# Kernel optimization log

Measured on AMD Instinct MI355X. Metric: run time of the kernel, lower is better.

The kernel has to match this reference:

```python
import jax, jax.numpy as jnp
import numpy as np

EPS = 1e-5
QB = 127.0  # 2**(8-1) - 1


def absmean_quantize(w):
    """Ternary quantization (BitNet b1.58): gamma = mean|W|, W_q in {-1,0,1}."""
    gamma = jnp.mean(jnp.abs(w))
    u = w / jnp.maximum(gamma, EPS)
    w_q = jnp.clip(jnp.round(u), -1.0, 1.0)
    return w_q, gamma


def absmax_quantize(x, bits=8):
    """Per-token int8 absmax quantization: alpha = max|x| over last dim."""
    qb = float(2 ** (bits - 1) - 1)
    alpha = jnp.max(jnp.abs(x), axis=-1, keepdims=True)  # [..., 1]
    u = x * qb / jnp.maximum(alpha, EPS)
    x_q = jnp.clip(jnp.round(u), -qb, qb)
    return x_q, alpha


def setup_inputs() -> dict:
    key = jax.random.key(0)
    k1, k2 = jax.random.split(key)
    B, S, D_IN, D_OUT = 4, 2048, 2048, 8192
    x = jax.random.normal(k1, (B, S, D_IN), dtype=jnp.float32)
    # kaiming-uniform-ish init scale for weight [out, in]
    bound = 1.0 / np.sqrt(D_IN)
    weight = jax.random.uniform(k2, (D_OUT, D_IN), minval=-bound, maxval=bound, dtype=jnp.float32)
    return {"x": x, "weight": weight}


def reference(x, weight):
    w_q, gamma = absmean_quantize(weight)          # [O,I], scalar
    x_q, alpha = absmax_quantize(x, bits=8)        # [B,S,I], [B,S,1]
    out = jnp.einsum('bsi,oi->bso', x_q, w_q)      # float matmul of quantized values
    scale = alpha * gamma / QB                     # [B,S,1]
    return out * scale
```

## Files before the change

### kernel.cpp

```cpp
#include <hip/hip_runtime.h>
#include <hip/hip_bf16.h>
#include <stdint.h>

typedef int i32x4 __attribute__((ext_vector_type(4)));

#define K_DIM 2048
#define M_DIM 8192
#define N_DIM 8192
#define QBF   127.0f
#define EPSF  1e-5f
#define NT    32

__device__ __forceinline__ void load_lds16(const void* gsrc, void* ldst) {
    __builtin_amdgcn_global_load_lds(
        (__attribute__((address_space(1))) void*)gsrc,
        (__attribute__((address_space(3))) void*)ldst,
        16, 0, 0);
}

__global__ __launch_bounds__(256) void k_abs_partial(const float* __restrict__ w,
                                                     float* __restrict__ partial) {
    __shared__ float red[256];
    int t = threadIdx.x, b = blockIdx.x;
    const float4* w4 = (const float4*)w;
    size_t base = (size_t)b * 2048;
    float s = 0.f;
#pragma unroll
    for (int j = 0; j < 8; ++j) {
        float4 v = w4[base + j * 256 + t];
        s += fabsf(v.x) + fabsf(v.y) + fabsf(v.z) + fabsf(v.w);
    }
    red[t] = s; __syncthreads();
    for (int off = 128; off > 0; off >>= 1) {
        if (t < off) red[t] += red[t + off];
        __syncthreads();
    }
    if (t == 0) partial[b] = red[0];
}

__global__ __launch_bounds__(256) void k_gamma(const float* __restrict__ partial,
                                               float* __restrict__ gamma) {
    __shared__ float red[256];
    int t = threadIdx.x;
    float s = 0.f;
#pragma unroll
    for (int j = 0; j < 8; ++j) s += partial[t + j * 256];
    red[t] = s; __syncthreads();
    for (int off = 128; off > 0; off >>= 1) {
        if (t < off) red[t] += red[t + off];
        __syncthreads();
    }
    if (t == 0) gamma[0] = red[0] / 16777216.0f;
}

__global__ __launch_bounds__(256) void k_quant_w(const float* __restrict__ w,
                                                 const float* __restrict__ gamma,
                                                 uint* __restrict__ wq) {
    float g = fmaxf(gamma[0], EPSF);
    int tid = blockIdx.x * 256 + threadIdx.x;
    float4 v = ((const float4*)w)[tid];
    int a = (int)fminf(fmaxf(rintf(v.x / g), -1.f), 1.f);
    int b = (int)fminf(fmaxf(rintf(v.y / g), -1.f), 1.f);
    int c = (int)fminf(fmaxf(rintf(v.z / g), -1.f), 1.f);
    int d = (int)fminf(fmaxf(rintf(v.w / g), -1.f), 1.f);
    wq[tid] = (a & 255) | ((b & 255) << 8) | ((c & 255) << 16) | ((d & 255) << 24);
}

__global__ __launch_bounds__(256) void k_quant_x(const float* __restrict__ x,
                                                 uint* __restrict__ xq,
                                                 float* __restrict__ alpha) {
    __shared__ float red[256];
    int t = threadIdx.x, row = blockIdx.x;
    const float4* x4 = (const float4*)x + (size_t)row * 512;
    float4 v0 = x4[t], v1 = x4[t + 256];
    float m = fmaxf(fmaxf(fabsf(v0.x), fabsf(v0.y)), fmaxf(fabsf(v0.z), fabsf(v0.w)));
    m = fmaxf(m, fmaxf(fmaxf(fabsf(v1.x), fabsf(v1.y)), fmaxf(fabsf(v1.z), fabsf(v1.w))));
    red[t] = m; __syncthreads();
    for (int off = 128; off > 0; off >>= 1) {
        if (t < off) red[t] = fmaxf(red[t], red[t + off]);
        __syncthreads();
    }
    float a = red[0];
    if (t == 0) alpha[row] = a;
    float den = fmaxf(a, EPSF);
    uint* q = xq + (size_t)row * 512;
    int q0 = (int)fminf(fmaxf(rintf(v0.x * QBF / den), -QBF), QBF);
    int q1 = (int)fminf(fmaxf(rintf(v0.y * QBF / den), -QBF), QBF);
    int q2 = (int)fminf(fmaxf(rintf(v0.z * QBF / den), -QBF), QBF);
    int q3 = (int)fminf(fmaxf(rintf(v0.w * QBF / den), -QBF), QBF);
    q[t] = (q0 & 255) | ((q1 & 255) << 8) | ((q2 & 255) << 16) | ((q3 & 255) << 24);
    q0 = (int)fminf(fmaxf(rintf(v1.x * QBF / den), -QBF), QBF);
    q1 = (int)fminf(fmaxf(rintf(v1.y * QBF / den), -QBF), QBF);
    q2 = (int)fminf(fmaxf(rintf(v1.z * QBF / den), -QBF), QBF);
    q3 = (int)fminf(fmaxf(rintf(v1.w * QBF / den), -QBF), QBF);
    q[t + 256] = (q0 & 255) | ((q1 & 255) << 8) | ((q2 & 255) << 16) | ((q3 & 255) << 24);
}

__global__ __launch_bounds__(256, 2) void k_gemm(const uint8_t* __restrict__ xq,
                                                 const uint8_t* __restrict__ wq,
                                                 const float* __restrict__ alpha,
                                                 const float* __restrict__ gamma,
                                                 float* __restrict__ out) {
    __shared__ __align__(16) char smem[73728];

    int bid = blockIdx.x;
    int wg = (bid & 7) * 256 + (bid >> 3);
    int tm = wg >> 6, tn = wg & 63;

    int t = threadIdx.x;
    int w = t >> 6, l = t & 63;
    int wr = w >> 1, wc = w & 1;

    const uint8_t* srcb[6];
    int dstq[6];
    {
        int rsub = l >> 2;
        int clog = (l & 3) ^ ((rsub >> 1) & 3);
#pragma unroll
        for (int j = 0; j < 6; ++j) {
            int q = w * 6 + j;
            int isB = q >> 4;
            int r = (isB ? (q & 7) : q) * 16 + rsub;
            int grow = isB ? tn * 128 + r : tm * 256 + r;
            srcb[j] = (isB ? wq : xq) + (size_t)grow * K_DIM + clog * 16;
            dstq[j] = q * 1024;
        }
    }

    i32x4 acc[8][4];
#pragma unroll
    for (int m = 0; m < 8; ++m)
#pragma unroll
        for (int n = 0; n < 4; ++n) acc[m][n] = (i32x4){0, 0, 0, 0};

    int lrow = l & 15, kgrp = l >> 4;
    int cph = (kgrp ^ ((lrow >> 1) & 3)) * 16;
    int aoff[8], boff[4];
#pragma unroll
    for (int mf = 0; mf < 8; ++mf) aoff[mf] = (wr * 128 + mf * 16 + lrow) * 64 + cph;
#pragma unroll
    for (int nf = 0; nf < 4; ++nf) boff[nf] = 16384 + (wc * 64 + nf * 16 + lrow) * 64 + cph;

#pragma unroll
    for (int p = 0; p < 2; ++p)
#pragma unroll
        for (int j = 0; j < 6; ++j)
            load_lds16(srcb[j] + (size_t)p * 64, smem + p * 24576 + dstq[j]);

    int slot = 0;
    for (int kt = 0; kt < NT; ++kt) {
        char* sb = smem + slot * 24576;
        if (kt < NT - 1) asm volatile("s_waitcnt vmcnt(6)" ::: "memory");
        else             asm volatile("s_waitcnt vmcnt(0)" ::: "memory");
        __builtin_amdgcn_s_barrier();

        i32x4 a[8], b[4];
#pragma unroll
        for (int mf = 0; mf < 4; ++mf) a[mf] = *(const i32x4*)(sb + aoff[mf]);
#pragma unroll
        for (int nf = 0; nf < 4; ++nf) b[nf] = *(const i32x4*)(sb + boff[nf]);
        __builtin_amdgcn_sched_barrier(0);
        if (kt + 2 < NT) {
            int ds = slot + 2; if (ds >= 3) ds -= 3;
            char* db = smem + ds * 24576;
#pragma unroll
            for (int j = 0; j < 6; ++j)
                load_lds16(srcb[j] + (size_t)(kt + 2) * 64, db + dstq[j]);
        }
        __builtin_amdgcn_sched_barrier(0);
#pragma unroll
        for (int mf = 4; mf < 8; ++mf) a[mf] = *(const i32x4*)(sb + aoff[mf]);

        asm volatile("s_waitcnt lgkmcnt(4)" ::: "memory");
        __builtin_amdgcn_sched_barrier(0);
        __builtin_amdgcn_s_setprio(1);
#pragma unroll
        for (int mf = 0; mf < 4; ++mf)
#pragma unroll
            for (int nf = 0; nf < 4; ++nf)
                acc[mf][nf] = __builtin_amdgcn_mfma_i32_16x16x64_i8(
                    a[mf], b[nf], acc[mf][nf], 0, 0, 0);
        __builtin_amdgcn_s_setprio(0);

        asm volatile("s_waitcnt lgkmcnt(0)" ::: "memory");
        __builtin_amdgcn_sched_barrier(0);
        __builtin_amdgcn_s_setprio(1);
#pragma unroll
        for (int mf = 4; mf < 8; ++mf)
#pragma unroll
            for (int nf = 0; nf < 4; ++nf)
                acc[mf][nf] = __builtin_amdgcn_mfma_i32_16x16x64_i8(
                    a[mf], b[nf], acc[mf][nf], 0, 0, 0);
        __builtin_amdgcn_s_setprio(0);

        slot = (slot == 2) ? 0 : slot + 1;
    }

    float gs = gamma[0] / QBF;
    int orow0 = tm * 256 + wr * 128 + kgrp * 4;
    int ocol = tn * 128 + wc * 64 + lrow;
#pragma unroll
    for (int mf = 0; mf < 8; ++mf)
#pragma unroll
        for (int r = 0; r < 4; ++r) {
            int row = orow0 + mf * 16 + r;
            float s = alpha[row] * gs;
            size_t rb = (size_t)row * N_DIM + ocol;
#pragma unroll
            for (int nf = 0; nf < 4; ++nf)
                out[rb + nf * 16] = (float)acc[mf][nf][r] * s;
        }
}

extern "C" void kernel_launch(void* const* d_in, const int* in_sizes, int n_in,
                              void* d_out, int out_size, void* d_ws, size_t ws_size,
                              hipStream_t stream) {
    const float* x  = (const float*)d_in[0];
    const float* wt = (const float*)d_in[1];
    float* out = (float*)d_out;

    char* ws = (char*)d_ws;
    uint8_t* xq     = (uint8_t*)ws;
    uint8_t* wq     = (uint8_t*)(ws + 16777216);
    float* alpha    = (float*)(ws + 33554432);
    float* partial  = (float*)(ws + 33587200);
    float* gamma    = (float*)(ws + 33595392);

    k_abs_partial<<<2048, 256, 0, stream>>>(wt, partial);
    k_gamma<<<1, 256, 0, stream>>>(partial, gamma);
    k_quant_w<<<16384, 256, 0, stream>>>(wt, gamma, (uint*)wq);
    k_quant_x<<<8192, 256, 0, stream>>>(x, (uint*)xq, alpha);
    k_gemm<<<2048, 256, 0, stream>>>(xq, wq, alpha, gamma, out);
}
```

Before: 222.1 us.

## Prefetch next k-tile LDS fragments into registers during current MFMAs

After: 221.1 us, median of 3. Within noise of the previous version (-0.5%).

```diff
diff --git a/kernel.cpp b/kernel.cpp
--- a/kernel.cpp
+++ b/kernel.cpp
@@ -141,60 +141,81 @@
 #pragma unroll
     for (int nf = 0; nf < 4; ++nf) boff[nf] = 16384 + (wc * 64 + nf * 16 + lrow) * 64 + cph;
 
+    i32x4 ALe[4], BBe[4], ALo[4], BBo[4], AH[4];
+
 #pragma unroll
     for (int p = 0; p < 2; ++p)
 #pragma unroll
         for (int j = 0; j < 6; ++j)
             load_lds16(srcb[j] + (size_t)p * 64, smem + p * 24576 + dstq[j]);
-
-    int slot = 0;
-    for (int kt = 0; kt < NT; ++kt) {
-        char* sb = smem + slot * 24576;
-        if (kt < NT - 1) asm volatile("s_waitcnt vmcnt(6)" ::: "memory");
-        else             asm volatile("s_waitcnt vmcnt(0)" ::: "memory");
-        __builtin_amdgcn_s_barrier();
-
-        i32x4 a[8], b[4];
-#pragma unroll
-        for (int mf = 0; mf < 4; ++mf) a[mf] = *(const i32x4*)(sb + aoff[mf]);
-#pragma unroll
-        for (int nf = 0; nf < 4; ++nf) b[nf] = *(const i32x4*)(sb + boff[nf]);
-        __builtin_amdgcn_sched_barrier(0);
-        if (kt + 2 < NT) {
-            int ds = slot + 2; if (ds >= 3) ds -= 3;
-            char* db = smem + ds * 24576;
-#pragma unroll
-            for (int j = 0; j < 6; ++j)
-                load_lds16(srcb[j] + (size_t)(kt + 2) * 64, db + dstq[j]);
-        }
-        __builtin_amdgcn_sched_barrier(0);
-#pragma unroll
-        for (int mf = 4; mf < 8; ++mf) a[mf] = *(const i32x4*)(sb + aoff[mf]);
-
-        asm volatile("s_waitcnt lgkmcnt(4)" ::: "memory");
-        __builtin_amdgcn_sched_barrier(0);
-        __builtin_amdgcn_s_setprio(1);
-#pragma unroll
-        for (int mf = 0; mf < 4; ++mf)
-#pragma unroll
-            for (int nf = 0; nf < 4; ++nf)
-                acc[mf][nf] = __builtin_amdgcn_mfma_i32_16x16x64_i8(
-                    a[mf], b[nf], acc[mf][nf], 0, 0, 0);
-        __builtin_amdgcn_s_setprio(0);
-
-        asm volatile("s_waitcnt lgkmcnt(0)" ::: "memory");
-        __builtin_amdgcn_sched_barrier(0);
-        __builtin_amdgcn_s_setprio(1);
-#pragma unroll
-        for (int mf = 4; mf < 8; ++mf)
-#pragma unroll
-            for (int nf = 0; nf < 4; ++nf)
-                acc[mf][nf] = __builtin_amdgcn_mfma_i32_16x16x64_i8(
-                    a[mf], b[nf], acc[mf][nf], 0, 0, 0);
-        __builtin_amdgcn_s_setprio(0);
-
-        slot = (slot == 2) ? 0 : slot + 1;
-    }
+    asm volatile("s_waitcnt vmcnt(6)" ::: "memory");
+    __builtin_amdgcn_s_barrier();
+#pragma unroll
+    for (int mf = 0; mf < 4; ++mf) ALe[mf] = *(const i32x4*)(smem + aoff[mf]);
+#pragma unroll
+    for (int nf = 0; nf < 4; ++nf) BBe[nf] = *(const i32x4*)(smem + boff[nf]);
+    asm volatile("s_waitcnt lgkmcnt(0)" ::: "memory");
+    __builtin_amdgcn_sched_barrier(0);
+
+    int sl = 0;
+
+#define ITER(KT, ALC, BBC, ALN, BBN)                                         \
+    {                                                                        \
+        asm volatile("s_waitcnt vmcnt(0)" ::: "memory");    \
+        __builtin_amdgcn_s_barrier();                                        \
+        int s1 = sl + 1; if (s1 >= 3) s1 = 0;                                \
+        int s2 = s1 + 1; if (s2 >= 3) s2 = 0;                                \
+        char* sb  = smem + sl * 24576;                                       \
+        char* sbn = smem + s1 * 24576;                                       \
+        if ((KT) + 2 < NT) {                                                 \
+            char* db = smem + s2 * 24576;                                    \
+            _Pragma("unroll")                                                \
+            for (int j = 0; j < 6; ++j)                                      \
+                load_lds16(srcb[j] + (size_t)((KT) + 2) * 64, db + dstq[j]); \
+        }                                                                    \
+        _Pragma("unroll")                                                    \
+        for (int mf = 0; mf < 4; ++mf)                                       \
+            AH[mf] = *(const i32x4*)(sb + aoff[mf + 4]);                     \
+        if ((KT) + 1 < NT) {                                                 \
+            _Pragma("unroll")                                                \
+            for (int mf = 0; mf < 4; ++mf)                                   \
+                ALN[mf] = *(const i32x4*)(sbn + aoff[mf]);                   \
+            _Pragma("unroll")                                                \
+            for (int nf = 0; nf < 4; ++nf)                                   \
+                BBN[nf] = *(const i32x4*)(sbn + boff[nf]);                   \
+        }                                                                    \
+        __builtin_amdgcn_sched_barrier(0);                                   \
+        __builtin_amdgcn_s_setprio(1);                                       \
+        _Pragma("unroll")                                                    \
+        for (int mf = 0; mf < 4; ++mf)                                       \
+            _Pragma("unroll")                                                \
+            for (int nf = 0; nf < 4; ++nf)                                   \
+                acc[mf][nf] = __builtin_amdgcn_mfma_i32_16x16x64_i8(         \
+                    ALC[mf], BBC[nf], acc[mf][nf], 0, 0, 0);                 \
+        __builtin_amdgcn_s_setprio(0);                                       \
+        if ((KT) + 1 < NT)                                                   \
+            asm volatile("s_waitcnt lgkmcnt(8)" ::: "memory");               \
+        else                                                                 \
+            asm volatile("s_waitcnt lgkmcnt(0)" ::: "memory");               \
+        __builtin_amdgcn_sched_barrier(0);                                   \
+        __builtin_amdgcn_s_setprio(1);                                       \
+        _Pragma("unroll")                                                    \
+        for (int mf = 0; mf < 4; ++mf)                                       \
+            _Pragma("unroll")                                                \
+            for (int nf = 0; nf < 4; ++nf)                                   \
+                acc[mf + 4][nf] = __builtin_amdgcn_mfma_i32_16x16x64_i8(     \
+                    AH[mf], BBC[nf], acc[mf + 4][nf], 0, 0, 0);              \
+        __builtin_amdgcn_s_setprio(0);                                       \
+        asm volatile("s_waitcnt lgkmcnt(0)" ::: "memory");   \
+        __builtin_amdgcn_sched_barrier(0);                                   \
+        sl = s1;                                                             \
+    }
+
+    for (int kt = 0; kt < NT; kt += 2) {
+        ITER(kt,     ALe, BBe, ALo, BBo)
+        ITER(kt + 1, ALo, BBo, ALe, BBe)
+    }
+#undef ITER
 
     float gs = gamma[0] / QBF;
     int orow0 = tm * 256 + wr * 128 + kgrp * 4;
```

## Enlarge GEMM tile to 256x256 with per-wave private LDS double buffering

Applied to the files above, without the earlier changes.

Measured after the change: 220.5 us. Within noise of the previous version (-0.7%).

```diff
diff --git a/kernel.cpp b/kernel.cpp
--- a/kernel.cpp
+++ b/kernel.cpp
@@ -96,82 +96,80 @@
     q[t + 256] = (q0 & 255) | ((q1 & 255) << 8) | ((q2 & 255) << 16) | ((q3 & 255) << 24);
 }
 
-__global__ __launch_bounds__(256, 2) void k_gemm(const uint8_t* __restrict__ xq,
+__global__ __launch_bounds__(256, 1) void k_gemm(const uint8_t* __restrict__ xq,
                                                  const uint8_t* __restrict__ wq,
                                                  const float* __restrict__ alpha,
                                                  const float* __restrict__ gamma,
                                                  float* __restrict__ out) {
-    __shared__ __align__(16) char smem[73728];
+    __shared__ __align__(16) char smem[131072];
 
     int bid = blockIdx.x;
-    int wg = (bid & 7) * 256 + (bid >> 3);
-    int tm = wg >> 6, tn = wg & 63;
+    int wg = (bid & 7) * 128 + (bid >> 3);
+    int tm = wg >> 5, tn = wg & 31;
 
     int t = threadIdx.x;
     int w = t >> 6, l = t & 63;
     int wr = w >> 1, wc = w & 1;
-
-    const uint8_t* srcb[6];
-    int dstq[6];
+    char* wbase = smem + w * 32768;
+
+    const uint8_t* srcb[16];
     {
         int rsub = l >> 2;
         int clog = (l & 3) ^ ((rsub >> 1) & 3);
 #pragma unroll
-        for (int j = 0; j < 6; ++j) {
-            int q = w * 6 + j;
-            int isB = q >> 4;
-            int r = (isB ? (q & 7) : q) * 16 + rsub;
-            int grow = isB ? tn * 128 + r : tm * 256 + r;
+        for (int j = 0; j < 16; ++j) {
+            int isB = j >> 3;
+            int r = (j & 7) * 16 + rsub;
+            int grow = isB ? tn * 256 + wc * 128 + r
+                           : tm * 256 + wr * 128 + r;
             srcb[j] = (isB ? wq : xq) + (size_t)grow * K_DIM + clog * 16;
-            dstq[j] = q * 1024;
         }
     }
 
-    i32x4 acc[8][4];
+    i32x4 acc[8][8];
 #pragma unroll
     for (int m = 0; m < 8; ++m)
 #pragma unroll
-        for (int n = 0; n < 4; ++n) acc[m][n] = (i32x4){0, 0, 0, 0};
+        for (int n = 0; n < 8; ++n) acc[m][n] = (i32x4){0, 0, 0, 0};
 
     int lrow = l & 15, kgrp = l >> 4;
     int cph = (kgrp ^ ((lrow >> 1) & 3)) * 16;
-    int aoff[8], boff[4];
-#pragma unroll
-    for (int mf = 0; mf < 8; ++mf) aoff[mf] = (wr * 128 + mf * 16 + lrow) * 64 + cph;
-#pragma unroll
-    for (int nf = 0; nf < 4; ++nf) boff[nf] = 16384 + (wc * 64 + nf * 16 + lrow) * 64 + cph;
-
-#pragma unroll
-    for (int p = 0; p < 2; ++p)
-#pragma unroll
-        for (int j = 0; j < 6; ++j)
-            load_lds16(srcb[j] + (size_t)p * 64, smem + p * 24576 + dstq[j]);
-
-    int slot = 0;
-    for (int kt = 0; kt < NT; ++kt) {
-        char* sb = smem + slot * 24576;
-        if (kt < NT - 1) asm volatile("s_waitcnt vmcnt(6)" ::: "memory");
-        else             asm volatile("s_waitcnt vmcnt(0)" ::: "memory");
-        __builtin_amdgcn_s_barrier();
-
-        i32x4 a[8], b[4];
+    int aoff[8], boff[8];
+#pragma unroll
+    for (int mf = 0; mf < 8; ++mf) aoff[mf] = (mf * 16 + lrow) * 64 + cph;
+#pragma unroll
+    for (int nf = 0; nf < 8; ++nf) boff[nf] = 8192 + (nf * 16 + lrow) * 64 + cph;
+
+#pragma unroll
+    for (int j = 0; j < 16; ++j)
+        load_lds16(srcb[j], wbase + j * 1024);
+
+    for (int s = 0; s < NT; ++s) {
+        char* sb = wbase + (s & 1) * 16384;
+        if (s + 1 < NT) {
+            char* db = wbase + ((s + 1) & 1) * 16384;
+#pragma unroll
+            for (int j = 0; j < 16; ++j)
+                load_lds16(srcb[j] + (size_t)(s + 1) * 64, db + j * 1024);
+            asm volatile("s_waitcnt vmcnt(16)" ::: "memory");
+        } else {
+            asm volatile("s_waitcnt vmcnt(0)" ::: "memory");
+        }
+        __builtin_amdgcn_sched_barrier(0);
+
+        i32x4 a[8], b[8];
+#pragma unroll
+        for (int nf = 0; nf < 4; ++nf) b[nf] = *(const i32x4*)(sb + boff[nf]);
 #pragma unroll
         for (int mf = 0; mf < 4; ++mf) a[mf] = *(const i32x4*)(sb + aoff[mf]);
-#pragma unroll
-        for (int nf = 0; nf < 4; ++nf) b[nf] = *(const i32x4*)(sb + boff[nf]);
-        __builtin_amdgcn_sched_barrier(0);
-        if (kt + 2 < NT) {
-            int ds = slot + 2; if (ds >= 3) ds -= 3;
-            char* db = smem + ds * 24576;
-#pragma unroll
-            for (int j = 0; j < 6; ++j)
-                load_lds16(srcb[j] + (size_t)(kt + 2) * 64, db + dstq[j]);
-        }
         __builtin_amdgcn_sched_barrier(0);
 #pragma unroll
         for (int mf = 4; mf < 8; ++mf) a[mf] = *(const i32x4*)(sb + aoff[mf]);
-
-        asm volatile("s_waitcnt lgkmcnt(4)" ::: "memory");
+        __builtin_amdgcn_sched_barrier(0);
+#pragma unroll
+        for (int nf = 4; nf < 8; ++nf) b[nf] = *(const i32x4*)(sb + boff[nf]);
+
+        asm volatile("s_waitcnt lgkmcnt(8)" ::: "memory");
         __builtin_amdgcn_sched_barrier(0);
         __builtin_amdgcn_s_setprio(1);
 #pragma unroll
@@ -182,7 +180,7 @@
                     a[mf], b[nf], acc[mf][nf], 0, 0, 0);
         __builtin_amdgcn_s_setprio(0);
 
-        asm volatile("s_waitcnt lgkmcnt(0)" ::: "memory");
+        asm volatile("s_waitcnt lgkmcnt(4)" ::: "memory");
         __builtin_amdgcn_sched_barrier(0);
         __builtin_amdgcn_s_setprio(1);
 #pragma unroll
@@ -193,22 +191,32 @@
                     a[mf], b[nf], acc[mf][nf], 0, 0, 0);
         __builtin_amdgcn_s_setprio(0);
 
-        slot = (slot == 2) ? 0 : slot + 1;
+        asm volatile("s_waitcnt lgkmcnt(0)" ::: "memory");
+        __builtin_amdgcn_sched_barrier(0);
+        __builtin_amdgcn_s_setprio(1);
+#pragma unroll
+        for (int mf = 0; mf < 8; ++mf)
+#pragma unroll
+            for (int nf = 4; nf < 8; ++nf)
+                acc[mf][nf] = __builtin_amdgcn_mfma_i32_16x16x64_i8(
+                    a[mf], b[nf], acc[mf][nf], 0, 0, 0);
+        __builtin_amdgcn_s_setprio(0);
     }
 
     float gs = gamma[0] / QBF;
     int orow0 = tm * 256 + wr * 128 + kgrp * 4;
-    int ocol = tn * 128 + wc * 64 + lrow;
+    int ocol0 = tn * 256 + wc * 128 + lrow;
 #pragma unroll
     for (int mf = 0; mf < 8; ++mf)
 #pragma unroll
         for (int r = 0; r < 4; ++r) {
             int row = orow0 + mf * 16 + r;
             float s = alpha[row] * gs;
-            size_t rb = (size_t)row * N_DIM + ocol;
-#pragma unroll
-            for (int nf = 0; nf < 4; ++nf)
-                out[rb + nf * 16] = (float)acc[mf][nf][r] * s;
+            size_t rb = (size_t)row * N_DIM + ocol0;
+#pragma unroll
+            for (int nf = 0; nf < 8; ++nf)
+                __builtin_nontemporal_store((float)acc[mf][nf][r] * s,
+                                            out + rb + nf * 16);
         }
 }
 
@@ -230,5 +238,5 @@
     k_gamma<<<1, 256, 0, stream>>>(partial, gamma);
     k_quant_w<<<16384, 256, 0, stream>>>(wt, gamma, (uint*)wq);
     k_quant_x<<<8192, 256, 0, stream>>>(x, (uint*)xq, alpha);
-    k_gemm<<<2048, 256, 0, stream>>>(xq, wq, alpha, gamma, out);
-}
+    k_gemm<<<1024, 256, 0, stream>>>(xq, wq, alpha, gamma, out);
+}
```
